# Optimization experiments

Measured on AMD Instinct MI355X. Metric: run time of the kernel, lower is better.

## Reference

```python
import jax, jax.numpy as jnp
import numpy as np
from jax import lax

# dims
B, N, D, H, K, NS = 16, 4096, 64, 128, 32, 1024  # clouds, pts/cloud, feat, hidden, max neighbors, fps samples
R = 0.2  # radius


def _fps(pos, n_s):
    """Farthest point sampling on one cloud. pos: [N,3] -> idx [n_s] int32."""
    n = pos.shape[0]

    def step(carry, _):
        dist, last = carry
        d = jnp.sum((pos - pos[last]) ** 2, axis=-1)
        dist = jnp.minimum(dist, d)
        nxt = jnp.argmax(dist).astype(jnp.int32)
        return (dist, nxt), last

    init = (jnp.full((n,), 1e10, pos.dtype), jnp.int32(0))
    _, idx = lax.scan(step, init, None, length=n_s)
    return idx


def setup_inputs() -> dict:
    key = jax.random.key(0)
    ks = jax.random.split(key, 6)
    s1 = 1.0 / np.sqrt(D + 1)
    s2 = 1.0 / np.sqrt(H)
    s3 = 1.0 / np.sqrt(D + H)
    return {
        "x": jax.random.normal(ks[0], (B, N, D), jnp.float32),
        "pos": jax.random.uniform(ks[1], (B, N, 3), jnp.float32),
        "W1": jax.random.normal(ks[2], (D + 1, H), jnp.float32) * s1,
        "b1": jnp.zeros((H,), jnp.float32),
        "W2": jax.random.normal(ks[3], (H, 3), jnp.float32) * s2,
        "b2": jnp.zeros((3,), jnp.float32),
        "W3": jax.random.normal(ks[4], (D + H, H), jnp.float32) * s3,
        "b3": jnp.zeros((H,), jnp.float32),
    }


def reference(x, pos, W1, b1, W2, b2, W3, b3):
    # 1) FPS downsample per cloud -> centers
    idx = jax.vmap(lambda p: _fps(p, NS))(pos)                    # [B,NS]
    pos_s = jax.vmap(lambda p, i: p[i])(pos, idx)                 # [B,NS,3]

    # 2) radius neighbor search: nearest-K within R (<= max_num_neighbors=32)
    d2 = jnp.sum((pos_s[:, :, None, :] - pos[:, None, :, :]) ** 2, axis=-1)  # [B,NS,N]
    masked = jnp.where(d2 <= R * R, d2, jnp.inf)
    neg, nbr = lax.top_k(-masked, K)                              # nearest K
    valid = (-neg) <= R * R                                       # [B,NS,K]

    # 3) gather neighbor features/positions
    x_j = jax.vmap(lambda a, i: a[i])(x, nbr)                     # [B,NS,K,D]
    pos_j = jax.vmap(lambda a, i: a[i])(pos, nbr)                 # [B,NS,K,3]
    diff = pos_j - pos_s[:, :, None, :]                           # pos_j - pos_i
    d2sel = jnp.sum(diff ** 2, axis=-1)
    dist = jnp.where(d2sel > 0, jnp.sqrt(jnp.where(d2sel > 0, d2sel, 1.0)), 0.0)

    # 4) message MLPs
    feat = jnp.concatenate([x_j, dist[..., None]], axis=-1)       # [B,NS,K,D+1]
    emb = jax.nn.relu(feat @ W1 + b1)                             # nn_msg_x
    pw = emb @ W2 + b2                                            # nn_msg_pos
    pmsg = diff * pw

    # 5) masked aggregate: sum for x, mean for pos
    m = valid[..., None].astype(emb.dtype)
    aggr_x = jnp.sum(emb * m, axis=2)                             # [B,NS,H]
    cnt = jnp.maximum(jnp.sum(m, axis=2), 1.0)                    # [B,NS,1]
    aggr_pos = jnp.sum(pmsg * m, axis=2) / cnt                    # [B,NS,3]

    # 6) update
    x_d = jax.vmap(lambda a, i: a[i])(x, idx)                     # [B,NS,D]
    out_x = jax.nn.relu(jnp.concatenate([x_d, aggr_x], axis=-1) @ W3 + b3)
    out_pos = pos_s + aggr_pos
    return out_x, out_pos, idx
```

## Files before the change

### kernel.cpp

```cpp
#include <hip/hip_runtime.h>
#include <math.h>

#define B_ 16
#define N_ 4096
#define D_ 64
#define H_ 128
#define K_ 32
#define NS_ 1024
#define R2_ 0.04f
#define CAP_ 1024

typedef short short8 __attribute__((ext_vector_type(8)));
typedef float f32x4 __attribute__((ext_vector_type(4)));
typedef unsigned short ushort_t;

static __device__ __forceinline__ short f2bf(float f) {
    unsigned u = __float_as_uint(f);
    unsigned r = (u + 0x7FFFu + ((u >> 16) & 1u)) >> 16;
    return (short)r;
}

template<int CTRL, int RM>
static __device__ __forceinline__ unsigned dppmov(unsigned v) {
    return (unsigned)__builtin_amdgcn_update_dpp((int)v, (int)v, CTRL, RM, 0xF, false);
}

#define DPP_FMAX_STEP(CTRL, RM)                                           \
    {                                                                     \
        float n = __uint_as_float(dppmov<CTRL, RM>(__float_as_uint(wm))); \
        wm = fmaxf(wm, n);                                                \
    }

#define DPP_UMIN_STEP(CTRL, RM)                                           \
    {                                                                     \
        unsigned n = dppmov<CTRL, RM>(cand);                              \
        cand = n < cand ? n : cand;                                       \
    }

#define DPP_UMIN_STEP_V(var, CTRL, RM)                                    \
    {                                                                     \
        unsigned n = dppmov<CTRL, RM>(var);                               \
        var = n < var ? n : var;                                          \
    }

__global__ __launch_bounds__(256) void cvt_kernel(
    const float* __restrict__ x, ushort_t* __restrict__ xb)
{
    const size_t i = ((size_t)blockIdx.x * 256 + threadIdx.x) * 8;
    float4 a = *(const float4*)(x + i);
    float4 c = *(const float4*)(x + i + 4);
    short8 o;
    o[0] = f2bf(a.x); o[1] = f2bf(a.y); o[2] = f2bf(a.z); o[3] = f2bf(a.w);
    o[4] = f2bf(c.x); o[5] = f2bf(c.y); o[6] = f2bf(c.z); o[7] = f2bf(c.w);
    *(short8*)(xb + i) = o;
}

__global__ __launch_bounds__(256, 1) void fps_kernel(
    const float* __restrict__ pos, int* __restrict__ idx_i,
    float* __restrict__ idx_f, float* __restrict__ pos_s)
{
    __shared__ float4 lpos4[N_];
    __shared__ float4 sres[NS_];
    __shared__ unsigned long long skey[2][4];
    __shared__ float4 scoord[2][4];
    const int b = blockIdx.x;
    const int t = threadIdx.x;
    const int wv = t >> 6;
    const int lane = t & 63;
    const float* posb = pos + (size_t)b * N_ * 3;
    for (int p = t; p < N_; p += 256)
        lpos4[p] = make_float4(posb[3 * p + 0], posb[3 * p + 1], posb[3 * p + 2], 0.f);
    __syncthreads();

    float px[16], py[16], pz[16], dist[16];
#pragma unroll
    for (int j = 0; j < 16; ++j) {
        float4 v = lpos4[t + 256 * j];
        px[j] = v.x; py[j] = v.y; pz[j] = v.z;
        dist[j] = 1e10f;
    }
    unsigned curidx = 0;
    float4 c0 = lpos4[0];
    float ccx = c0.x, ccy = c0.y, ccz = c0.z;

    for (int ns = 0; ns < NS_; ++ns) {
        if (t == 0)
            sres[ns] = make_float4(ccx, ccy, ccz, __uint_as_float(curidx));
        float bv = -1.f; int bj = 0;
#pragma unroll
        for (int j = 0; j < 16; ++j) {
            float dx = __fsub_rn(px[j], ccx);
            float dy = __fsub_rn(py[j], ccy);
            float dz = __fsub_rn(pz[j], ccz);
            float d2 = __fadd_rn(__fadd_rn(__fmul_rn(dx, dx), __fmul_rn(dy, dy)), __fmul_rn(dz, dz));
            float dn = fminf(dist[j], d2);
            dist[j] = dn;
            bool g = dn > bv;
            bv = g ? dn : bv;
            bj = g ? j : bj;
        }
        float wm = bv;
        DPP_FMAX_STEP(0x111, 0xF)
        DPP_FMAX_STEP(0x112, 0xF)
        DPP_FMAX_STEP(0x114, 0xF)
        DPP_FMAX_STEP(0x118, 0xF)
        DPP_FMAX_STEP(0x142, 0xA)
        DPP_FMAX_STEP(0x143, 0xC)
        const float wavemax = __uint_as_float(
            (unsigned)__builtin_amdgcn_readlane((int)__float_as_uint(wm), 63));
        const unsigned pidx = (unsigned)t + ((unsigned)bj << 8);
        const unsigned long long mask = __ballot(bv == wavemax);
        unsigned widx;
        if (__popcll(mask) == 1) {
            const int wl = __ffsll((long long)mask) - 1;
            widx = (unsigned)__builtin_amdgcn_readlane((int)pidx, wl);
        } else {
            unsigned cand = (bv == wavemax) ? pidx : 0xFFFFFFFFu;
            DPP_UMIN_STEP(0x111, 0xF)
            DPP_UMIN_STEP(0x112, 0xF)
            DPP_UMIN_STEP(0x114, 0xF)
            DPP_UMIN_STEP(0x118, 0xF)
            DPP_UMIN_STEP(0x142, 0xA)
            DPP_UMIN_STEP(0x143, 0xC)
            widx = (unsigned)__builtin_amdgcn_readlane((int)cand, 63);
        }
        float4 wc = lpos4[widx];
        if (lane == 0) {
            skey[ns & 1][wv] = (((unsigned long long)__float_as_uint(wavemax)) << 32)
                             | (unsigned long long)(0xFFFFFFFFu - widx);
            scoord[ns & 1][wv] = wc;
        }
        __syncthreads();
        {
            unsigned sid = (unsigned)(lane & 3);
            unsigned long long skv = skey[ns & 1][sid];
            float4 scv = scoord[ns & 1][sid];
            unsigned kh2 = (unsigned)(skv >> 32), kl2 = (unsigned)skv;
#define SLOT_STEP(CTRL)                                                        \
            {                                                                  \
                unsigned nh = dppmov<CTRL, 0xF>(kh2);                          \
                unsigned nl = dppmov<CTRL, 0xF>(kl2);                          \
                unsigned nsid = dppmov<CTRL, 0xF>(sid);                        \
                unsigned long long nk = (((unsigned long long)nh) << 32) | nl; \
                unsigned long long ok = (((unsigned long long)kh2) << 32) | kl2;\
                if (nk > ok) { kh2 = nh; kl2 = nl; sid = nsid; }               \
            }
            SLOT_STEP(0x101)
            SLOT_STEP(0x102)
#undef SLOT_STEP
            const int slotwin = __builtin_amdgcn_readfirstlane((int)sid);
            curidx = 0xFFFFFFFFu - (unsigned)__builtin_amdgcn_readfirstlane((int)kl2);
            ccx = __uint_as_float((unsigned)__builtin_amdgcn_readlane(
                      (int)__float_as_uint(scv.x), slotwin));
            ccy = __uint_as_float((unsigned)__builtin_amdgcn_readlane(
                      (int)__float_as_uint(scv.y), slotwin));
            ccz = __uint_as_float((unsigned)__builtin_amdgcn_readlane(
                      (int)__float_as_uint(scv.z), slotwin));
        }
    }
    __syncthreads();
    for (int i = t; i < NS_; i += 256) {
        float4 r = sres[i];
        unsigned id = __float_as_uint(r.w);
        idx_i[b * NS_ + i] = (int)id;
        idx_f[b * NS_ + i] = (float)id;
        pos_s[(b * NS_ + i) * 3 + 0] = r.x;
        pos_s[(b * NS_ + i) * 3 + 1] = r.y;
        pos_s[(b * NS_ + i) * 3 + 2] = r.z;
    }
}

__global__ __launch_bounds__(256) void nbr_kernel(
    const float* __restrict__ pos, const float* __restrict__ pos_s,
    int* __restrict__ nbr, float* __restrict__ cntv)
{
    __shared__ unsigned long long ck[4][CAP_];
    const int w = threadIdx.x >> 6;
    const int lane = threadIdx.x & 63;
    const int s = blockIdx.x * 4 + w;
    const int b = s >> 10;
    const float cx = pos_s[s * 3 + 0], cy = pos_s[s * 3 + 1], cz = pos_s[s * 3 + 2];
    const float* posb = pos + (size_t)b * N_ * 3;
    int m = 0;
    for (int base = 0; base < N_; base += 64) {
        int p = base + lane;
        float dx = __fsub_rn(posb[3 * p + 0], cx);
        float dy = __fsub_rn(posb[3 * p + 1], cy);
        float dz = __fsub_rn(posb[3 * p + 2], cz);
        float d2 = __fadd_rn(__fadd_rn(__fmul_rn(dx, dx), __fmul_rn(dy, dy)), __fmul_rn(dz, dz));
        bool in = (d2 <= R2_);
        unsigned long long msk = __ballot(in);
        int before = __popcll(msk & ((1ull << lane) - 1ull));
        int slot = m + before;
        if (in && slot < CAP_)
            ck[w][slot] = ((unsigned long long)__float_as_uint(d2) << 32) | (unsigned)p;
        m += __popcll(msk);
    }
    if (m > CAP_) m = CAP_;
    __asm__ volatile("s_waitcnt lgkmcnt(0)" ::: "memory");
    int kcnt = m < K_ ? m : K_;
    if (m <= 256) {
        unsigned long long kr[4];
#pragma unroll
        for (int r = 0; r < 4; ++r) {
            int q = r * 64 + lane;
            unsigned long long v = ck[w][q & (CAP_ - 1)];
            kr[r] = (q < m) ? v : ~0ull;
        }
        unsigned chosen = 0;
        for (int k = 0; k < kcnt; ++k) {
            unsigned long long localk = ~0ull; int br = -1;
#pragma unroll
            for (int r = 0; r < 4; ++r) {
                bool ok = (!((chosen >> r) & 1u)) && (kr[r] < localk);
                localk = ok ? kr[r] : localk;
                br = ok ? r : br;
            }
            const unsigned mybits = (unsigned)(localk >> 32);
            const unsigned myidx = (unsigned)localk;
            unsigned wb = mybits;
            DPP_UMIN_STEP_V(wb, 0x111, 0xF)
            DPP_UMIN_STEP_V(wb, 0x112, 0xF)
            DPP_UMIN_STEP_V(wb, 0x114, 0xF)
            DPP_UMIN_STEP_V(wb, 0x118, 0xF)
            DPP_UMIN_STEP_V(wb, 0x142, 0xA)
            DPP_UMIN_STEP_V(wb, 0x143, 0xC)
            const unsigned minbits = (unsigned)__builtin_amdgcn_readlane((int)wb, 63);
            const unsigned long long wmask = __ballot(mybits == minbits);
            unsigned widx;
            if (__popcll(wmask) == 1) {
                const int wl = __ffsll((long long)wmask) - 1;
                widx = (unsigned)__builtin_amdgcn_readlane((int)myidx, wl);
            } else {
                unsigned cand = (mybits == minbits) ? myidx : 0xFFFFFFFFu;
                DPP_UMIN_STEP(0x111, 0xF)
                DPP_UMIN_STEP(0x112, 0xF)
                DPP_UMIN_STEP(0x114, 0xF)
                DPP_UMIN_STEP(0x118, 0xF)
                DPP_UMIN_STEP(0x142, 0xA)
                DPP_UMIN_STEP(0x143, 0xC)
                widx = (unsigned)__builtin_amdgcn_readlane((int)cand, 63);
            }
            if (mybits == minbits && myidx == widx) chosen |= 1u << br;
            if (lane == 0) nbr[s * K_ + k] = (int)widx;
        }
    } else {
        unsigned chosen = 0;
        for (int k = 0; k < kcnt; ++k) {
            unsigned long long localk = ~0ull; int bslot = -1;
            for (int r = 0; r * 64 + lane < m; ++r) {
                if (chosen & (1u << r)) continue;
                int q = r * 64 + lane;
                unsigned long long key = ck[w][q];
                if (key < localk) { localk = key; bslot = q; }
            }
            unsigned kh = (unsigned)(localk >> 32), kl = (unsigned)localk;
#define DPP_MIN_STEP2(CTRL, RM)                                           \
            {                                                             \
                unsigned nh = dppmov<CTRL, RM>(kh);                       \
                unsigned nl = dppmov<CTRL, RM>(kl);                       \
                unsigned long long nk = (((unsigned long long)nh) << 32) | nl; \
                unsigned long long ok = (((unsigned long long)kh) << 32) | kl; \
                if (nk < ok) { kh = nh; kl = nl; }                        \
            }
            DPP_MIN_STEP2(0x111, 0xF)
            DPP_MIN_STEP2(0x112, 0xF)
            DPP_MIN_STEP2(0x114, 0xF)
            DPP_MIN_STEP2(0x118, 0xF)
            DPP_MIN_STEP2(0x142, 0xA)
            DPP_MIN_STEP2(0x143, 0xC)
#undef DPP_MIN_STEP2
            unsigned mh = (unsigned)__builtin_amdgcn_readlane((int)kh, 63);
            unsigned ml = (unsigned)__builtin_amdgcn_readlane((int)kl, 63);
            unsigned long long bk = (((unsigned long long)mh) << 32) | ml;
            if (localk == bk && bslot >= 0) chosen |= 1u << (bslot >> 6);
            if (lane == 0) nbr[s * K_ + k] = (int)(bk & 0xFFFFFFFFull);
        }
    }
    if (lane == 0) {
        for (int k = kcnt; k < K_; ++k) nbr[s * K_ + k] = -1;
        cntv[s] = (float)kcnt;
    }
}

__global__ __launch_bounds__(256) void msg_kernel(
    const ushort_t* __restrict__ xb, const float* __restrict__ pos,
    const float* __restrict__ W1, const float* __restrict__ b1,
    const float* __restrict__ W2, const float* __restrict__ b2,
    const float* __restrict__ pos_s, const int* __restrict__ nbr,
    const float* __restrict__ cntv, float* __restrict__ aggr_x,
    float* __restrict__ out_pos)
{
    __shared__ __align__(16) char smem[4 * 5120];
    const int t = threadIdx.x;
    const int wv = t >> 6, lane = t & 63;
    const int quad = lane >> 4, cl = lane & 15;
    char* wb = smem + wv * 5120;

    short8 bfrag[8][2];
    float b1v[8], w1dv[8], w2v0[8], w2v1[8], w2v2[8];
#pragma unroll
    for (int Nt = 0; Nt < 8; ++Nt) {
        const int h = Nt * 16 + cl;
#pragma unroll
        for (int ks = 0; ks < 2; ++ks) {
            short8 f;
#pragma unroll
            for (int jj = 0; jj < 8; ++jj)
                f[jj] = f2bf(W1[(ks * 32 + quad * 8 + jj) * H_ + h]);
            bfrag[Nt][ks] = f;
        }
        b1v[Nt] = b1[h];
        w1dv[Nt] = W1[64 * H_ + h];
        w2v0[Nt] = W2[h * 3 + 0];
        w2v1[Nt] = W2[h * 3 + 1];
        w2v2[Nt] = W2[h * 3 + 2];
    }
    const float b20 = b2[0], b21 = b2[1], b22 = b2[2];

    const int kkg = lane >> 1, half = lane & 1;
    for (int i = 0; i < 4; ++i) {
        const int s = blockIdx.x * 16 + wv * 4 + i;
        const int b = s >> 10;
        const int n = nbr[s * K_ + kkg];
        {
            char* frow = wb + kkg * 144 + half * 64;
            if (n >= 0) {
                const short8* xr = (const short8*)(xb + ((size_t)b * N_ + n) * D_) + half * 4;
#pragma unroll
                for (int q = 0; q < 4; ++q) *(short8*)(frow + q * 16) = xr[q];
            } else {
                short8 z = {0, 0, 0, 0, 0, 0, 0, 0};
#pragma unroll
                for (int q = 0; q < 4; ++q) *(short8*)(frow + q * 16) = z;
            }
            if (half == 0) {
                float dxm = 0.f, dym = 0.f, dzm = 0.f, de = -1.f;
                if (n >= 0) {
                    const float* pj = pos + ((size_t)b * N_ + n) * 3;
                    float dx = pj[0] - pos_s[s * 3 + 0];
                    float dy = pj[1] - pos_s[s * 3 + 1];
                    float dz = pj[2] - pos_s[s * 3 + 2];
                    float d2 = dx * dx + dy * dy + dz * dz;
                    de = d2 > 0.f ? sqrtf(d2) : 0.f;
                    dxm = dx; dym = dy; dzm = dz;
                }
                f32x4 sv = {dxm, dym, dzm, de};
                *(f32x4*)(wb + 4608 + kkg * 16) = sv;
            }
        }
        float agp[8] = {0, 0, 0, 0, 0, 0, 0, 0};
        float gp0[8] = {0, 0, 0, 0, 0, 0, 0, 0};
        float gp1[8] = {0, 0, 0, 0, 0, 0, 0, 0};
        float gp2[8] = {0, 0, 0, 0, 0, 0, 0, 0};
#pragma unroll
        for (int Mt = 0; Mt < 2; ++Mt) {
            short8 a0 = *(short8*)(wb + (Mt * 16 + cl) * 144 + quad * 16);
            short8 a1 = *(short8*)(wb + (Mt * 16 + cl) * 144 + 64 + quad * 16);
            f32x4 acc[8];
#pragma unroll
            for (int Nt = 0; Nt < 8; ++Nt) {
                f32x4 z = {0.f, 0.f, 0.f, 0.f};
                z = __builtin_amdgcn_mfma_f32_16x16x32_bf16(a0, bfrag[Nt][0], z, 0, 0, 0);
                z = __builtin_amdgcn_mfma_f32_16x16x32_bf16(a1, bfrag[Nt][1], z, 0, 0, 0);
                acc[Nt] = z;
            }
            f32x4 sd[4];
#pragma unroll
            for (int r = 0; r < 4; ++r)
                sd[r] = *(f32x4*)(wb + 4608 + (Mt * 16 + quad * 4 + r) * 16);
#pragma unroll
            for (int Nt = 0; Nt < 8; ++Nt) {
#pragma unroll
                for (int r = 0; r < 4; ++r) {
                    float dr = sd[r][3];
                    float wgt = dr >= 0.f ? 1.f : 0.f;
                    float dd = dr >= 0.f ? dr : 0.f;
                    float e = fmaf(dd, w1dv[Nt], acc[Nt][r]) + b1v[Nt];
                    e = e > 0.f ? e : 0.f;
                    agp[Nt] = fmaf(wgt, e, agp[Nt]);
                    gp0[Nt] = fmaf(sd[r][0], e, gp0[Nt]);
                    gp1[Nt] = fmaf(sd[r][1], e, gp1[Nt]);
                    gp2[Nt] = fmaf(sd[r][2], e, gp2[Nt]);
                }
            }
        }
#pragma unroll
        for (int Nt = 0; Nt < 8; ++Nt) {
            float v = agp[Nt]; v += __shfl_xor(v, 16); v += __shfl_xor(v, 32);
            aggr_x[(size_t)s * H_ + Nt * 16 + cl] = v;
            float g0 = gp0[Nt]; g0 += __shfl_xor(g0, 16); g0 += __shfl_xor(g0, 32); gp0[Nt] = g0;
            float g1 = gp1[Nt]; g1 += __shfl_xor(g1, 16); g1 += __shfl_xor(g1, 32); gp1[Nt] = g1;
            float g2 = gp2[Nt]; g2 += __shfl_xor(g2, 16); g2 += __shfl_xor(g2, 32); gp2[Nt] = g2;
        }
        float pr0 = 0.f, pr1 = 0.f, pr2 = 0.f;
#pragma unroll
        for (int Nt = 0; Nt < 8; ++Nt) {
            pr0 = fmaf(w2v0[Nt], gp0[Nt], pr0);
            pr1 = fmaf(w2v1[Nt], gp1[Nt], pr1);
            pr2 = fmaf(w2v2[Nt], gp2[Nt], pr2);
        }
#pragma unroll
        for (int off = 1; off < 16; off <<= 1) {
            pr0 += __shfl_xor(pr0, off);
            pr1 += __shfl_xor(pr1, off);
            pr2 += __shfl_xor(pr2, off);
        }
        f32x4 dsv = *(f32x4*)(wb + 4608 + (lane & 31) * 16);
        float q0 = dsv[0], q1 = dsv[1], q2 = dsv[2];
#pragma unroll
        for (int off = 1; off < 32; off <<= 1) {
            q0 += __shfl_xor(q0, off);
            q1 += __shfl_xor(q1, off);
            q2 += __shfl_xor(q2, off);
        }
        float cnt = cntv[s]; if (cnt < 1.f) cnt = 1.f;
        if (lane < 3) {
            float pr = lane == 0 ? pr0 : (lane == 1 ? pr1 : pr2);
            float qq = lane == 0 ? q0 : (lane == 1 ? q1 : q2);
            float bb = lane == 0 ? b20 : (lane == 1 ? b21 : b22);
            out_pos[s * 3 + lane] = pos_s[s * 3 + lane] + (pr + bb * qq) / cnt;
        }
    }
}

__global__ __launch_bounds__(128) void out_kernel(
    const float* __restrict__ x, const float* __restrict__ W3,
    const float* __restrict__ b3, const int* __restrict__ idx_i,
    const float* __restrict__ aggr_x, float* __restrict__ out_x)
{
    __shared__ float rows[32][208];
    const int t = threadIdx.x;
    const int s0 = blockIdx.x * 32;
    const int sl = t >> 2, part = t & 3;
    const int s = s0 + sl;
    const int b = s >> 10;
    const int id = idx_i[s];
    {
        const float4* xr = (const float4*)(x + ((size_t)b * N_ + id) * D_);
        float4* rr = (float4*)&rows[sl][0];
#pragma unroll
        for (int q = 0; q < 4; ++q) rr[part * 4 + q] = xr[part * 4 + q];
        const float4* ar = (const float4*)(aggr_x + (size_t)s * H_);
        float4* rr2 = (float4*)&rows[sl][64];
#pragma unroll
        for (int q = 0; q < 8; ++q) rr2[part * 8 + q] = ar[part * 8 + q];
    }
    __syncthreads();
    float acc[32];
#pragma unroll
    for (int i = 0; i < 32; ++i) acc[i] = 0.f;
    for (int j4 = 0; j4 < 48; ++j4) {
        float w0 = W3[(j4 * 4 + 0) * H_ + t];
        float w1 = W3[(j4 * 4 + 1) * H_ + t];
        float w2 = W3[(j4 * 4 + 2) * H_ + t];
        float w3 = W3[(j4 * 4 + 3) * H_ + t];
#pragma unroll
        for (int i = 0; i < 32; ++i) {
            const float4 f = *(const float4*)&rows[i][j4 * 4];
            float a = acc[i];
            a = fmaf(f.x, w0, a); a = fmaf(f.y, w1, a);
            a = fmaf(f.z, w2, a); a = fmaf(f.w, w3, a);
            acc[i] = a;
        }
    }
    const float bb = b3[t];
#pragma unroll
    for (int i = 0; i < 32; ++i) {
        float v = acc[i] + bb;
        v = v > 0.f ? v : 0.f;
        out_x[(size_t)(s0 + i) * H_ + t] = v;
    }
}

extern "C" void kernel_launch(void* const* d_in, const int* in_sizes, int n_in,
                              void* d_out, int out_size, void* d_ws, size_t ws_size,
                              hipStream_t stream) {
    const float* x   = (const float*)d_in[0];
    const float* pos = (const float*)d_in[1];
    const float* W1  = (const float*)d_in[2];
    const float* b1  = (const float*)d_in[3];
    const float* W2  = (const float*)d_in[4];
    const float* b2  = (const float*)d_in[5];
    const float* W3  = (const float*)d_in[6];
    const float* b3  = (const float*)d_in[7];

    float* out_x   = (float*)d_out;
    float* out_pos = (float*)d_out + 2097152;
    float* idx_f   = (float*)d_out + 2146304;

    char* ws = (char*)d_ws;
    int*      idx_i  = (int*)ws;
    float*    pos_s  = (float*)(ws + 65536);
    int*      nbr    = (int*)(ws + 262144);
    float*    cntv   = (float*)(ws + 2359296);
    float*    aggr_x = (float*)(ws + 2424832);
    ushort_t* x_bf16 = (ushort_t*)(ws + 10813440);

    cvt_kernel<<<(B_ * N_ * D_) / (256 * 8), 256, 0, stream>>>(x, x_bf16);
    fps_kernel<<<B_, 256, 0, stream>>>(pos, idx_i, idx_f, pos_s);
    nbr_kernel<<<(B_ * NS_) / 4, 256, 0, stream>>>(pos, pos_s, nbr, cntv);
    msg_kernel<<<(B_ * NS_) / 16, 256, 0, stream>>>(x_bf16, pos, W1, b1, W2, b2,
                                                    pos_s, nbr, cntv, aggr_x, out_pos);
    out_kernel<<<(B_ * NS_) / 32, 128, 0, stream>>>(x, W3, b3, idx_i, aggr_x, out_x);
}
```

Measured before the change: 970.1 us.

## Widen FPS to 1024 threads and carry winner coords in registers

```diff
diff --git a/kernel.cpp b/kernel.cpp
--- a/kernel.cpp
+++ b/kernel.cpp
@@ -55,40 +55,38 @@
     *(short8*)(xb + i) = o;
 }
 
-__global__ __launch_bounds__(256, 1) void fps_kernel(
+__global__ __launch_bounds__(1024, 1) void fps_kernel(
     const float* __restrict__ pos, int* __restrict__ idx_i,
     float* __restrict__ idx_f, float* __restrict__ pos_s)
 {
-    __shared__ float4 lpos4[N_];
     __shared__ float4 sres[NS_];
-    __shared__ unsigned long long skey[2][4];
-    __shared__ float4 scoord[2][4];
+    __shared__ unsigned long long skey[2][16];
+    __shared__ float4 scoord[2][16];
     const int b = blockIdx.x;
     const int t = threadIdx.x;
     const int wv = t >> 6;
     const int lane = t & 63;
     const float* posb = pos + (size_t)b * N_ * 3;
-    for (int p = t; p < N_; p += 256)
-        lpos4[p] = make_float4(posb[3 * p + 0], posb[3 * p + 1], posb[3 * p + 2], 0.f);
-    __syncthreads();
-
-    float px[16], py[16], pz[16], dist[16];
-#pragma unroll
-    for (int j = 0; j < 16; ++j) {
-        float4 v = lpos4[t + 256 * j];
-        px[j] = v.x; py[j] = v.y; pz[j] = v.z;
+
+    float px[4], py[4], pz[4], dist[4];
+#pragma unroll
+    for (int j = 0; j < 4; ++j) {
+        const int p = t + 1024 * j;
+        px[j] = posb[3 * p + 0];
+        py[j] = posb[3 * p + 1];
+        pz[j] = posb[3 * p + 2];
         dist[j] = 1e10f;
     }
     unsigned curidx = 0;
-    float4 c0 = lpos4[0];
-    float ccx = c0.x, ccy = c0.y, ccz = c0.z;
+    float ccx = posb[0], ccy = posb[1], ccz = posb[2];
 
     for (int ns = 0; ns < NS_; ++ns) {
         if (t == 0)
             sres[ns] = make_float4(ccx, ccy, ccz, __uint_as_float(curidx));
         float bv = -1.f; int bj = 0;
-#pragma unroll
-        for (int j = 0; j < 16; ++j) {
+        float bx = px[0], by = py[0], bz = pz[0];
+#pragma unroll
+        for (int j = 0; j < 4; ++j) {
             float dx = __fsub_rn(px[j], ccx);
             float dy = __fsub_rn(py[j], ccy);
             float dz = __fsub_rn(pz[j], ccz);
@@ -98,6 +96,9 @@
             bool g = dn > bv;
             bv = g ? dn : bv;
             bj = g ? j : bj;
+            bx = g ? px[j] : bx;
+            by = g ? py[j] : by;
+            bz = g ? pz[j] : bz;
         }
         float wm = bv;
         DPP_FMAX_STEP(0x111, 0xF)
@@ -108,12 +109,16 @@
         DPP_FMAX_STEP(0x143, 0xC)
         const float wavemax = __uint_as_float(
             (unsigned)__builtin_amdgcn_readlane((int)__float_as_uint(wm), 63));
-        const unsigned pidx = (unsigned)t + ((unsigned)bj << 8);
+        const unsigned pidx = (unsigned)t + ((unsigned)bj << 10);
         const unsigned long long mask = __ballot(bv == wavemax);
         unsigned widx;
+        float wx, wy, wz;
         if (__popcll(mask) == 1) {
             const int wl = __ffsll((long long)mask) - 1;
             widx = (unsigned)__builtin_amdgcn_readlane((int)pidx, wl);
+            wx = __uint_as_float((unsigned)__builtin_amdgcn_readlane((int)__float_as_uint(bx), wl));
+            wy = __uint_as_float((unsigned)__builtin_amdgcn_readlane((int)__float_as_uint(by), wl));
+            wz = __uint_as_float((unsigned)__builtin_amdgcn_readlane((int)__float_as_uint(bz), wl));
         } else {
             unsigned cand = (bv == wavemax) ? pidx : 0xFFFFFFFFu;
             DPP_UMIN_STEP(0x111, 0xF)
@@ -123,16 +128,20 @@
             DPP_UMIN_STEP(0x142, 0xA)
             DPP_UMIN_STEP(0x143, 0xC)
             widx = (unsigned)__builtin_amdgcn_readlane((int)cand, 63);
-        }
-        float4 wc = lpos4[widx];
+            const unsigned long long m2 = __ballot((bv == wavemax) && (pidx == widx));
+            const int wl2 = __ffsll((long long)m2) - 1;
+            wx = __uint_as_float((unsigned)__builtin_amdgcn_readlane((int)__float_as_uint(bx), wl2));
+            wy = __uint_as_float((unsigned)__builtin_amdgcn_readlane((int)__float_as_uint(by), wl2));
+            wz = __uint_as_float((unsigned)__builtin_amdgcn_readlane((int)__float_as_uint(bz), wl2));
+        }
         if (lane == 0) {
             skey[ns & 1][wv] = (((unsigned long long)__float_as_uint(wavemax)) << 32)
                              | (unsigned long long)(0xFFFFFFFFu - widx);
-            scoord[ns & 1][wv] = wc;
+            scoord[ns & 1][wv] = make_float4(wx, wy, wz, 0.f);
         }
         __syncthreads();
         {
-            unsigned sid = (unsigned)(lane & 3);
+            unsigned sid = (unsigned)(lane & 15);
             unsigned long long skv = skey[ns & 1][sid];
             float4 scv = scoord[ns & 1][sid];
             unsigned kh2 = (unsigned)(skv >> 32), kl2 = (unsigned)skv;
@@ -147,6 +156,8 @@
             }
             SLOT_STEP(0x101)
             SLOT_STEP(0x102)
+            SLOT_STEP(0x104)
+            SLOT_STEP(0x108)
 #undef SLOT_STEP
             const int slotwin = __builtin_amdgcn_readfirstlane((int)sid);
             curidx = 0xFFFFFFFFu - (unsigned)__builtin_amdgcn_readfirstlane((int)kl2);
@@ -159,7 +170,7 @@
         }
     }
     __syncthreads();
-    for (int i = t; i < NS_; i += 256) {
+    for (int i = t; i < NS_; i += 1024) {
         float4 r = sres[i];
         unsigned id = __float_as_uint(r.w);
         idx_i[b * NS_ + i] = (int)id;
@@ -498,7 +509,7 @@
     ushort_t* x_bf16 = (ushort_t*)(ws + 10813440);
 
     cvt_kernel<<<(B_ * N_ * D_) / (256 * 8), 256, 0, stream>>>(x, x_bf16);
-    fps_kernel<<<B_, 256, 0, stream>>>(pos, idx_i, idx_f, pos_s);
+    fps_kernel<<<B_, 1024, 0, stream>>>(pos, idx_i, idx_f, pos_s);
     nbr_kernel<<<(B_ * NS_) / 4, 256, 0, stream>>>(pos, pos_s, nbr, cntv);
     msg_kernel<<<(B_ * NS_) / 16, 256, 0, stream>>>(x_bf16, pos, W1, b1, W2, b2,
                                                     pos_s, nbr, cntv, aggr_x, out_pos);
```

Result: slower. 1.444 ms (+48.9%).

## Restructure FPS reduction using LDS atomicMax key and register-tracked winner coords

Applied to the files above, without the earlier changes.

```diff
diff --git a/kernel.cpp b/kernel.cpp
--- a/kernel.cpp
+++ b/kernel.cpp
@@ -29,6 +29,12 @@
     {                                                                     \
         float n = __uint_as_float(dppmov<CTRL, RM>(__float_as_uint(wm))); \
         wm = fmaxf(wm, n);                                                \
+    }
+
+#define DPP_UMAX_STEP(CTRL, RM)                                           \
+    {                                                                     \
+        unsigned n = dppmov<CTRL, RM>(cand);                              \
+        cand = n > cand ? n : cand;                                       \
     }
 
 #define DPP_UMIN_STEP(CTRL, RM)                                           \
@@ -59,34 +65,38 @@
     const float* __restrict__ pos, int* __restrict__ idx_i,
     float* __restrict__ idx_f, float* __restrict__ pos_s)
 {
-    __shared__ float4 lpos4[N_];
-    __shared__ float4 sres[NS_];
-    __shared__ unsigned long long skey[2][4];
     __shared__ float4 scoord[2][4];
+    __shared__ unsigned long long cell[3];
     const int b = blockIdx.x;
     const int t = threadIdx.x;
     const int wv = t >> 6;
     const int lane = t & 63;
     const float* posb = pos + (size_t)b * N_ * 3;
-    for (int p = t; p < N_; p += 256)
-        lpos4[p] = make_float4(posb[3 * p + 0], posb[3 * p + 1], posb[3 * p + 2], 0.f);
+
+    float px[16], py[16], pz[16], dist[16];
+#pragma unroll
+    for (int j = 0; j < 16; ++j) {
+        const int p = t + 256 * j;
+        px[j] = posb[3 * p + 0];
+        py[j] = posb[3 * p + 1];
+        pz[j] = posb[3 * p + 2];
+        dist[j] = 1e10f;
+    }
+    if (t < 3) cell[t] = 0ull;
+    float ccx = posb[0], ccy = posb[1], ccz = posb[2];
+    if (t == 0) {
+        idx_i[b * NS_ + 0] = 0;
+        idx_f[b * NS_ + 0] = 0.f;
+        pos_s[(b * NS_ + 0) * 3 + 0] = ccx;
+        pos_s[(b * NS_ + 0) * 3 + 1] = ccy;
+        pos_s[(b * NS_ + 0) * 3 + 2] = ccz;
+    }
     __syncthreads();
 
-    float px[16], py[16], pz[16], dist[16];
-#pragma unroll
-    for (int j = 0; j < 16; ++j) {
-        float4 v = lpos4[t + 256 * j];
-        px[j] = v.x; py[j] = v.y; pz[j] = v.z;
-        dist[j] = 1e10f;
-    }
-    unsigned curidx = 0;
-    float4 c0 = lpos4[0];
-    float ccx = c0.x, ccy = c0.y, ccz = c0.z;
-
-    for (int ns = 0; ns < NS_; ++ns) {
-        if (t == 0)
-            sres[ns] = make_float4(ccx, ccy, ccz, __uint_as_float(curidx));
+    int p = 1, pp = 0;
+    for (int ns = 1; ns < NS_; ++ns) {
         float bv = -1.f; int bj = 0;
+        float bx = px[0], by = py[0], bz = pz[0];
 #pragma unroll
         for (int j = 0; j < 16; ++j) {
             float dx = __fsub_rn(px[j], ccx);
@@ -98,6 +108,9 @@
             bool g = dn > bv;
             bv = g ? dn : bv;
             bj = g ? j : bj;
+            bx = g ? px[j] : bx;
+            by = g ? py[j] : by;
+            bz = g ? pz[j] : bz;
         }
         float wm = bv;
         DPP_FMAX_STEP(0x111, 0xF)
@@ -109,64 +122,48 @@
         const float wavemax = __uint_as_float(
             (unsigned)__builtin_amdgcn_readlane((int)__float_as_uint(wm), 63));
         const unsigned pidx = (unsigned)t + ((unsigned)bj << 8);
-        const unsigned long long mask = __ballot(bv == wavemax);
-        unsigned widx;
-        if (__popcll(mask) == 1) {
-            const int wl = __ffsll((long long)mask) - 1;
-            widx = (unsigned)__builtin_amdgcn_readlane((int)pidx, wl);
-        } else {
-            unsigned cand = (bv == wavemax) ? pidx : 0xFFFFFFFFu;
-            DPP_UMIN_STEP(0x111, 0xF)
-            DPP_UMIN_STEP(0x112, 0xF)
-            DPP_UMIN_STEP(0x114, 0xF)
-            DPP_UMIN_STEP(0x118, 0xF)
-            DPP_UMIN_STEP(0x142, 0xA)
-            DPP_UMIN_STEP(0x143, 0xC)
-            widx = (unsigned)__builtin_amdgcn_readlane((int)cand, 63);
-        }
-        float4 wc = lpos4[widx];
+        unsigned cand = (bv == wavemax) ? (4096u - pidx) : 0u;
+        DPP_UMAX_STEP(0x111, 0xF)
+        DPP_UMAX_STEP(0x112, 0xF)
+        DPP_UMAX_STEP(0x114, 0xF)
+        DPP_UMAX_STEP(0x118, 0xF)
+        DPP_UMAX_STEP(0x142, 0xA)
+        DPP_UMAX_STEP(0x143, 0xC)
+        const unsigned wcand = (unsigned)__builtin_amdgcn_readlane((int)cand, 63);
+        const unsigned widx = 4096u - wcand;
+        const int wl = (int)(widx & 63u);
+        if (lane == wl)
+            scoord[ns & 1][wv] = make_float4(bx, by, bz, 0.f);
         if (lane == 0) {
-            skey[ns & 1][wv] = (((unsigned long long)__float_as_uint(wavemax)) << 32)
-                             | (unsigned long long)(0xFFFFFFFFu - widx);
-            scoord[ns & 1][wv] = wc;
+            const unsigned long long key =
+                (((unsigned long long)__float_as_uint(wavemax)) << 32)
+                | (unsigned long long)wcand;
+            atomicMax(&cell[p], key);
         }
         __syncthreads();
-        {
-            unsigned sid = (unsigned)(lane & 3);
-            unsigned long long skv = skey[ns & 1][sid];
-            float4 scv = scoord[ns & 1][sid];
-            unsigned kh2 = (unsigned)(skv >> 32), kl2 = (unsigned)skv;
-#define SLOT_STEP(CTRL)                                                        \
-            {                                                                  \
-                unsigned nh = dppmov<CTRL, 0xF>(kh2);                          \
-                unsigned nl = dppmov<CTRL, 0xF>(kl2);                          \
-                unsigned nsid = dppmov<CTRL, 0xF>(sid);                        \
-                unsigned long long nk = (((unsigned long long)nh) << 32) | nl; \
-                unsigned long long ok = (((unsigned long long)kh2) << 32) | kl2;\
-                if (nk > ok) { kh2 = nh; kl2 = nl; sid = nsid; }               \
-            }
-            SLOT_STEP(0x101)
-            SLOT_STEP(0x102)
-#undef SLOT_STEP
-            const int slotwin = __builtin_amdgcn_readfirstlane((int)sid);
-            curidx = 0xFFFFFFFFu - (unsigned)__builtin_amdgcn_readfirstlane((int)kl2);
-            ccx = __uint_as_float((unsigned)__builtin_amdgcn_readlane(
-                      (int)__float_as_uint(scv.x), slotwin));
-            ccy = __uint_as_float((unsigned)__builtin_amdgcn_readlane(
-                      (int)__float_as_uint(scv.y), slotwin));
-            ccz = __uint_as_float((unsigned)__builtin_amdgcn_readlane(
-                      (int)__float_as_uint(scv.z), slotwin));
-        }
-    }
-    __syncthreads();
-    for (int i = t; i < NS_; i += 256) {
-        float4 r = sres[i];
-        unsigned id = __float_as_uint(r.w);
-        idx_i[b * NS_ + i] = (int)id;
-        idx_f[b * NS_ + i] = (float)id;
-        pos_s[(b * NS_ + i) * 3 + 0] = r.x;
-        pos_s[(b * NS_ + i) * 3 + 1] = r.y;
-        pos_s[(b * NS_ + i) * 3 + 2] = r.z;
+        const unsigned long long k = cell[p];
+        const float4 s0 = scoord[ns & 1][0];
+        const float4 s1 = scoord[ns & 1][1];
+        const float4 s2 = scoord[ns & 1][2];
+        const float4 s3 = scoord[ns & 1][3];
+        if (t == 0) cell[pp] = 0ull;
+        const unsigned curidx = 4096u - (unsigned)(k & 0xFFFFFFFFull);
+        const int wwin = (int)((curidx >> 6) & 3u);
+        const bool w1 = (wwin & 1) != 0, w2 = (wwin & 2) != 0;
+        float ax = w1 ? s1.x : s0.x, bx2 = w1 ? s3.x : s2.x;
+        float ay = w1 ? s1.y : s0.y, by2 = w1 ? s3.y : s2.y;
+        float az = w1 ? s1.z : s0.z, bz2 = w1 ? s3.z : s2.z;
+        ccx = w2 ? bx2 : ax;
+        ccy = w2 ? by2 : ay;
+        ccz = w2 ? bz2 : az;
+        if (t == 0) {
+            idx_i[b * NS_ + ns] = (int)curidx;
+            idx_f[b * NS_ + ns] = (float)curidx;
+            pos_s[(b * NS_ + ns) * 3 + 0] = ccx;
+            pos_s[(b * NS_ + ns) * 3 + 1] = ccy;
+            pos_s[(b * NS_ + ns) * 3 + 2] = ccz;
+        }
+        pp = p; p = (p == 2) ? 0 : p + 1;
     }
 }
 
```

After: 1.205 ms. +24.2%, slower.

## Fuse bf16 conversion into neighbor kernel and shrink candidate buffer

Applied to the files above, without the earlier changes.

```diff
diff --git a/kernel.cpp b/kernel.cpp
--- a/kernel.cpp
+++ b/kernel.cpp
@@ -8,7 +8,8 @@
 #define K_ 32
 #define NS_ 1024
 #define R2_ 0.04f
-#define CAP_ 1024
+#define NCAP_ 256
+#define NBR_GRID_ ((B_ * NS_) / 4)
 
 typedef short short8 __attribute__((ext_vector_type(8)));
 typedef float f32x4 __attribute__((ext_vector_type(4)));
@@ -42,18 +43,6 @@
         unsigned n = dppmov<CTRL, RM>(var);                               \
         var = n < var ? n : var;                                          \
     }
-
-__global__ __launch_bounds__(256) void cvt_kernel(
-    const float* __restrict__ x, ushort_t* __restrict__ xb)
-{
-    const size_t i = ((size_t)blockIdx.x * 256 + threadIdx.x) * 8;
-    float4 a = *(const float4*)(x + i);
-    float4 c = *(const float4*)(x + i + 4);
-    short8 o;
-    o[0] = f2bf(a.x); o[1] = f2bf(a.y); o[2] = f2bf(a.z); o[3] = f2bf(a.w);
-    o[4] = f2bf(c.x); o[5] = f2bf(c.y); o[6] = f2bf(c.z); o[7] = f2bf(c.w);
-    *(short8*)(xb + i) = o;
-}
 
 __global__ __launch_bounds__(256, 1) void fps_kernel(
     const float* __restrict__ pos, int* __restrict__ idx_i,
@@ -172,9 +161,20 @@
 
 __global__ __launch_bounds__(256) void nbr_kernel(
     const float* __restrict__ pos, const float* __restrict__ pos_s,
-    int* __restrict__ nbr, float* __restrict__ cntv)
+    int* __restrict__ nbr, float* __restrict__ cntv,
+    const float* __restrict__ x, ushort_t* __restrict__ xb)
 {
-    __shared__ unsigned long long ck[4][CAP_];
+    __shared__ unsigned long long ck[4][NCAP_];
+    if (blockIdx.x >= NBR_GRID_) {
+        const size_t i = ((size_t)(blockIdx.x - NBR_GRID_) * 256 + threadIdx.x) * 8;
+        float4 a = *(const float4*)(x + i);
+        float4 c = *(const float4*)(x + i + 4);
+        short8 o;
+        o[0] = f2bf(a.x); o[1] = f2bf(a.y); o[2] = f2bf(a.z); o[3] = f2bf(a.w);
+        o[4] = f2bf(c.x); o[5] = f2bf(c.y); o[6] = f2bf(c.z); o[7] = f2bf(c.w);
+        *(short8*)(xb + i) = o;
+        return;
+    }
     const int w = threadIdx.x >> 6;
     const int lane = threadIdx.x & 63;
     const int s = blockIdx.x * 4 + w;
@@ -192,19 +192,18 @@
         unsigned long long msk = __ballot(in);
         int before = __popcll(msk & ((1ull << lane) - 1ull));
         int slot = m + before;
-        if (in && slot < CAP_)
+        if (in && slot < NCAP_)
             ck[w][slot] = ((unsigned long long)__float_as_uint(d2) << 32) | (unsigned)p;
         m += __popcll(msk);
     }
-    if (m > CAP_) m = CAP_;
     __asm__ volatile("s_waitcnt lgkmcnt(0)" ::: "memory");
     int kcnt = m < K_ ? m : K_;
-    if (m <= 256) {
+    if (m <= NCAP_) {
         unsigned long long kr[4];
 #pragma unroll
         for (int r = 0; r < 4; ++r) {
             int q = r * 64 + lane;
-            unsigned long long v = ck[w][q & (CAP_ - 1)];
+            unsigned long long v = ck[w][q & (NCAP_ - 1)];
             kr[r] = (q < m) ? v : ~0ull;
         }
         unsigned chosen = 0;
@@ -245,14 +244,20 @@
             if (lane == 0) nbr[s * K_ + k] = (int)widx;
         }
     } else {
-        unsigned chosen = 0;
+        unsigned long long prev = 0ull;
         for (int k = 0; k < kcnt; ++k) {
-            unsigned long long localk = ~0ull; int bslot = -1;
-            for (int r = 0; r * 64 + lane < m; ++r) {
-                if (chosen & (1u << r)) continue;
-                int q = r * 64 + lane;
-                unsigned long long key = ck[w][q];
-                if (key < localk) { localk = key; bslot = q; }
+            unsigned long long localk = ~0ull;
+            for (int base = 0; base < N_; base += 64) {
+                int p = base + lane;
+                float dx = __fsub_rn(posb[3 * p + 0], cx);
+                float dy = __fsub_rn(posb[3 * p + 1], cy);
+                float dz = __fsub_rn(posb[3 * p + 2], cz);
+                float d2 = __fadd_rn(__fadd_rn(__fmul_rn(dx, dx), __fmul_rn(dy, dy)), __fmul_rn(dz, dz));
+                if (d2 <= R2_) {
+                    unsigned long long key =
+                        ((unsigned long long)__float_as_uint(d2) << 32) | (unsigned)p;
+                    if (key >= prev && key < localk) localk = key;
+                }
             }
             unsigned kh = (unsigned)(localk >> 32), kl = (unsigned)localk;
 #define DPP_MIN_STEP2(CTRL, RM)                                           \
@@ -273,7 +278,7 @@
             unsigned mh = (unsigned)__builtin_amdgcn_readlane((int)kh, 63);
             unsigned ml = (unsigned)__builtin_amdgcn_readlane((int)kl, 63);
             unsigned long long bk = (((unsigned long long)mh) << 32) | ml;
-            if (localk == bk && bslot >= 0) chosen |= 1u << (bslot >> 6);
+            prev = bk + 1ull;
             if (lane == 0) nbr[s * K_ + k] = (int)(bk & 0xFFFFFFFFull);
         }
     }
@@ -497,9 +502,9 @@
     float*    aggr_x = (float*)(ws + 2424832);
     ushort_t* x_bf16 = (ushort_t*)(ws + 10813440);
 
-    cvt_kernel<<<(B_ * N_ * D_) / (256 * 8), 256, 0, stream>>>(x, x_bf16);
     fps_kernel<<<B_, 256, 0, stream>>>(pos, idx_i, idx_f, pos_s);
-    nbr_kernel<<<(B_ * NS_) / 4, 256, 0, stream>>>(pos, pos_s, nbr, cntv);
+    nbr_kernel<<<NBR_GRID_ + (B_ * N_ * D_) / (256 * 8), 256, 0, stream>>>(
+        pos, pos_s, nbr, cntv, x, x_bf16);
     msg_kernel<<<(B_ * NS_) / 16, 256, 0, stream>>>(x_bf16, pos, W1, b1, W2, b2,
                                                     pos_s, nbr, cntv, aggr_x, out_pos);
     out_kernel<<<(B_ * NS_) / 32, 128, 0, stream>>>(x, W3, b3, idx_i, aggr_x, out_x);
```

Result: faster. 920.3 us (median of 3 runs) (-5.1%).
